# Kernel tuning notes

Hardware: AMD Instinct MI355X
Metric: run time of the kernel (lower is better)

## Reference

```python
import jax, jax.numpy as jnp
import numpy as np

TEMP = 1.75   # temp_schedule(epoch=5, warmup=10): 2.5 - 1.5*0.5
ALPHA = 0.5   # blend_schedule(epoch=5): 0.2 + 0.6*0.5
EPS = 1e-5
HEADS = 2


def _ln(x, g, b):
    mu = x.mean(-1, keepdims=True)
    var = ((x - mu) ** 2).mean(-1, keepdims=True)
    return (x - mu) * jax.lax.rsqrt(var + EPS) * g + b


def _gelu(x):
    return jax.nn.gelu(x, approximate=False)  # torch nn.GELU default = exact erf


def _attn_pool(x, ln_g, ln_b, in_w, in_b, out_w, out_b):
    # x: [N, T, E]; nn.MultiheadAttention self-attention then mean over T
    N, T, E = x.shape
    Dh = E // HEADS
    xn = _ln(x, ln_g, ln_b)
    qkv = xn @ in_w + in_b                      # [N, T, 3E] (in_w stored [E, 3E])
    q, k, v = jnp.split(qkv, 3, axis=-1)
    q = q.reshape(N, T, HEADS, Dh).transpose(0, 2, 1, 3)
    k = k.reshape(N, T, HEADS, Dh).transpose(0, 2, 1, 3)
    v = v.reshape(N, T, HEADS, Dh).transpose(0, 2, 1, 3)
    scores = jnp.einsum('nhqd,nhkd->nhqk', q, k) / jnp.sqrt(jnp.float32(Dh))
    a = jax.nn.softmax(scores, axis=-1)
    o = jnp.einsum('nhqk,nhkd->nhqd', a, v).transpose(0, 2, 1, 3).reshape(N, T, E)
    o = o @ out_w + out_b                       # [N, T, E]
    return o.mean(axis=1)                       # [N, E]


def setup_inputs() -> dict:
    key = jax.random.key(0)
    ks = iter(jax.random.split(key, 40))
    B, L, T, D = 4, 24, 400, 1024
    H = D // 2  # 512
    G = 4       # groups
    s = 0.02
    r = lambda shp: jax.random.normal(next(ks), shp, dtype=jnp.float32) * s
    inp = {
        'x': jax.random.normal(next(ks), (B, L, T, D), dtype=jnp.float32),
        'mlp_alpha': jnp.ones((L,), jnp.float32),
        # shared MLP: LN -> Linear(D,H) -> GELU -> Linear(H,H)
        's_ln_g': jnp.ones((D,), jnp.float32), 's_ln_b': jnp.zeros((D,), jnp.float32),
        's_w1': r((D, H)), 's_b1': jnp.zeros((H,), jnp.float32),
        's_w2': r((H, H)), 's_b2': jnp.zeros((H,), jnp.float32),
        # 4 group MLPs (stacked)
        'g_ln_g': jnp.ones((G, D), jnp.float32), 'g_ln_b': jnp.zeros((G, D), jnp.float32),
        'g_w1': r((G, D, H)), 'g_b1': jnp.zeros((G, H), jnp.float32),
        'g_w2': r((G, H, H)), 'g_b2': jnp.zeros((G, H), jnp.float32),
        # TimeAttentionPool (shared module): LN + MHA(512, 2 heads) + out_proj
        'p_ln_g': jnp.ones((H,), jnp.float32), 'p_ln_b': jnp.zeros((H,), jnp.float32),
        'p_in_w': r((H, 3 * H)), 'p_in_b': jnp.zeros((3 * H,), jnp.float32),
        'p_out_w': r((H, H)), 'p_out_b': jnp.zeros((H,), jnp.float32),
        # router: Linear(512,128) -> GELU -> Linear(128,1) -> sigmoid(/temp)
        'r_w1': r((H, 128)), 'r_b1': jnp.zeros((128,), jnp.float32),
        'r_w2': r((128, 1)), 'r_b2': jnp.zeros((1,), jnp.float32),
        # post norms
        'pn_g': jnp.ones((H,), jnp.float32), 'pn_b': jnp.zeros((H,), jnp.float32),
        'pnf_g': jnp.ones((H,), jnp.float32), 'pnf_b': jnp.zeros((H,), jnp.float32),
        # classifier 512 -> 256 -> 128 -> 2
        'c_w1': r((H, H // 2)), 'c_b1': jnp.zeros((H // 2,), jnp.float32),
        'c_w2': r((H // 2, H // 4)), 'c_b2': jnp.zeros((H // 4,), jnp.float32),
        'c_w3': r((H // 4, 2)), 'c_b3': jnp.zeros((2,), jnp.float32),
    }
    return inp


def reference(x, mlp_alpha, s_ln_g, s_ln_b, s_w1, s_b1, s_w2, s_b2,
              g_ln_g, g_ln_b, g_w1, g_b1, g_w2, g_b2,
              p_ln_g, p_ln_b, p_in_w, p_in_b, p_out_w, p_out_b,
              r_w1, r_b1, r_w2, r_b2, pn_g, pn_b, pnf_g, pnf_b,
              c_w1, c_b1, c_w2, c_b2, c_w3, c_b3):
    B, L, T, D = x.shape
    G = g_w1.shape[0]
    S = L // G  # group_size = 6; expert i uses group i // S
    H = s_w1.shape[1]

    # shared MLP over all experts at once (dropout inactive in eval)
    xs = _ln(x, s_ln_g, s_ln_b)                              # [B,L,T,D]
    shared = _gelu(xs @ s_w1 + s_b1) @ s_w2 + s_b2           # [B,L,T,H]

    # group MLPs: experts i//S -> group; reshape L -> (G, S)
    xg = x.reshape(B, G, S, T, D)
    xgn = _ln(xg, g_ln_g[:, None, None, :], g_ln_b[:, None, None, :])
    hg = _gelu(jnp.einsum('bgstd,gdh->bgsth', xgn, g_w1) + g_b1[None, :, None, None, :])
    grp = jnp.einsum('bgsth,ghk->bgstk', hg, g_w2) + g_b2[None, :, None, None, :]
    grp = grp.reshape(B, L, T, H)

    weighted = shared + mlp_alpha[None, :, None, None] * grp  # [B,L,T,H]

    # attn-pool every expert stream (fold L into batch)
    time_pooled = _attn_pool(weighted.reshape(B * L, T, H),
                             p_ln_g, p_ln_b, p_in_w, p_in_b, p_out_w, p_out_b)
    time_pooled = time_pooled.reshape(B, L, H)               # [B,L,H]

    # router
    rh = _gelu(time_pooled @ r_w1 + r_b1)
    logits_r = (rh @ r_w2 + r_b2)[..., 0]                    # [B,L]
    learned = jax.nn.sigmoid(logits_r / TEMP)
    routing_weights = ALPHA * learned + (1.0 - ALPHA) / L

    # soft fusion over experts
    fusion = (weighted * routing_weights[:, :, None, None]).sum(axis=1)  # [B,T,H]
    fusion = _ln(fusion, pn_g, pn_b).mean(axis=1)            # [B,H]

    shared_mean = shared.mean(axis=1)                        # [B,T,H]
    time_ctx = _attn_pool(shared_mean, p_ln_g, p_ln_b, p_in_w, p_in_b, p_out_w, p_out_b)

    fused_all = _ln(fusion, pnf_g, pnf_b) + _ln(time_ctx, pnf_g, pnf_b)  # [B,H]

    h = _gelu(fused_all @ c_w1 + c_b1)
    h = _gelu(h @ c_w2 + c_b2)
    logits = h @ c_w3 + c_b3                                 # [B,2]
    return logits, routing_weights, fused_all, time_pooled
```

## Files before the change

kernel.cpp:

```cpp
#include <hip/hip_runtime.h>
#include <stdint.h>


typedef float f32x4 __attribute__((ext_vector_type(4)));
typedef short bf16x8 __attribute__((ext_vector_type(8)));

__device__ __forceinline__ float bf2f(unsigned short u) {
  return __uint_as_float(((unsigned int)u) << 16);
}
__device__ __forceinline__ unsigned short f2bf(float f) {
  unsigned int u = __float_as_uint(f);
  u += 0x7fffu + ((u >> 16) & 1u);
  return (unsigned short)(u >> 16);
}
__device__ __forceinline__ float erf_fast(float x) {
  const float ax = fabsf(x);
  const float t = 1.0f / fmaf(0.3275911f, ax, 1.0f);
  float p = fmaf(1.061405429f, t, -1.453152027f);
  p = fmaf(p, t, 1.421413741f);
  p = fmaf(p, t, -0.284496736f);
  p = fmaf(p, t, 0.254829592f);
  const float e = __expf(-ax * ax);
  const float r = 1.0f - p * t * e;
  return copysignf(r, x);
}
__device__ __forceinline__ float gelu_f(float x) {
  return 0.5f * x * (1.0f + erf_fast(x * 0.70710678118654752440f));
}

typedef __attribute__((address_space(1))) const unsigned int gas_u32;
typedef __attribute__((address_space(3))) unsigned int las_u32;
__device__ __forceinline__ void gload16(const unsigned short* g, unsigned short* l) {
  __builtin_amdgcn_global_load_lds((gas_u32*)g, (las_u32*)l, 16, 0, 0);
}

template <int EPI, int GROUPED>
__global__ __launch_bounds__(256, 4) void gemm_bt(
    const unsigned short* __restrict__ A, const unsigned short* __restrict__ WT,
    const float* __restrict__ bias, unsigned short* __restrict__ Cout,
    const unsigned short* __restrict__ WT2, const float* __restrict__ bias2,
    const float* __restrict__ alpha_vec, unsigned short* __restrict__ vtbuf, int K,
    int N, int ldout, int Mslice) {
  const int tid = (int)threadIdx.x;
  const int w = tid >> 6, lane = tid & 63, g = lane >> 4, ql = lane & 15;
  const int wr = w >> 1, wc = w & 1;

  int bm, bn, z = 0;
  if (!GROUPED) {
    const int nbm = (int)gridDim.x, nbn = (int)gridDim.y;
    const int nb = nbm * nbn;
    const int lin = (int)blockIdx.x + nbm * (int)blockIdx.y;
    const int q = nb >> 3, r8 = nb & 7;
    const int xcd = lin & 7, c = lin >> 3;
    const int base = (xcd < r8) ? xcd * (q + 1) : r8 * (q + 1) + (xcd - r8) * q;
    const int widx = base + c;
    bm = widx / nbn;
    bn = widx - bm * nbn;
  } else {
    const int nbm = (int)gridDim.x, nbn = (int)gridDim.y;
    const int per_z = nbm * nbn;
    const int nb = per_z * (int)gridDim.z;
    const int lin =
        (int)blockIdx.x + nbm * ((int)blockIdx.y + (int)gridDim.y * (int)blockIdx.z);
    const int q = nb >> 3, r8 = nb & 7;
    const int xcd = lin & 7, c = lin >> 3;
    const int base = (xcd < r8) ? xcd * (q + 1) : r8 * (q + 1) + (xcd - r8) * q;
    const int widx = base + c;
    z = widx / per_z;
    const int rem = widx - z * per_z;
    bm = rem / nbn;
    bn = rem - bm * nbn;
  }
  const int n0 = bn * 128;

  int rowbase, rows_here;
  int nw0 = n0;
  const unsigned short* wt = WT;
  const float* bs = bias;
  if (GROUPED) {
    const int grp = z & 3;
    rowbase = z * Mslice + bm * 128;
    rows_here = Mslice - bm * 128;
    if (rows_here > 128) rows_here = 128;
    if (EPI == 4) {
      if (bn >= 4) {
        wt = WT2 + (size_t)grp * 512 * (size_t)K;
        bs = bias2 + (size_t)grp * 512;
        nw0 = n0 - 512;
      }
    } else if (EPI == 5) {
      wt = WT + (size_t)grp * (size_t)N * (size_t)K;
    } else {
      wt = WT + (size_t)grp * (size_t)N * (size_t)K;
      bs = bias + (size_t)grp * (size_t)N;
    }
  } else {
    rowbase = bm * 128;
    rows_here = Mslice - bm * 128;
    if (rows_here > 128) rows_here = 128;
  }

  __shared__ __align__(16) unsigned short sA[2][128 * 32];
  __shared__ __align__(16) unsigned short sB[2][128 * 32];

  f32x4 acc[4][4];
#pragma unroll
  for (int i = 0; i < 4; ++i)
#pragma unroll
    for (int j = 0; j < 4; ++j) acc[i][j] = (f32x4){0.f, 0.f, 0.f, 0.f};

  const int swzg = (lane & 3) ^ ((lane >> 3) & 3);
  const int rA0 = w * 32 + (lane >> 2);
  const int rA1 = rA0 + 16;
  const int rA0c = rA0 < rows_here ? rA0 : rows_here - 1;
  const int rA1c = rA1 < rows_here ? rA1 : rows_here - 1;
  const unsigned short* a0p = A + (size_t)(rowbase + rA0c) * K + swzg * 8;
  const unsigned short* a1p = A + (size_t)(rowbase + rA1c) * K + swzg * 8;
  const unsigned short* b0p = wt + (size_t)(nw0 + rA0) * K + swzg * 8;
  const unsigned short* b1p = wt + (size_t)(nw0 + rA1) * K + swzg * 8;
  const int ldsw = w * 1024;

  const int aroff = (wr * 64 + ql) * 32 + ((g ^ ((ql >> 1) & 3)) * 8);
  const int broff = (wc * 64 + ql) * 32 + ((g ^ ((ql >> 1) & 3)) * 8);

  const int nsteps = K >> 5;
  gload16(a0p, &sA[0][ldsw]);
  gload16(a1p, &sA[0][ldsw + 512]);
  gload16(b0p, &sB[0][ldsw]);
  gload16(b1p, &sB[0][ldsw + 512]);
  __syncthreads();

  for (int s = 0; s < nsteps; ++s) {
    const int cur = s & 1;
    if (s + 1 < nsteps) {
      const int k0 = (s + 1) << 5;
      const int nxt = cur ^ 1;
      gload16(a0p + k0, &sA[nxt][ldsw]);
      gload16(a1p + k0, &sA[nxt][ldsw + 512]);
      gload16(b0p + k0, &sB[nxt][ldsw]);
      gload16(b1p + k0, &sB[nxt][ldsw + 512]);
    }
    bf16x8 af[4], bfr[4];
#pragma unroll
    for (int mi = 0; mi < 4; ++mi)
      af[mi] = *(const bf16x8*)(&sA[cur][aroff + mi * 512]);
#pragma unroll
    for (int ni = 0; ni < 4; ++ni)
      bfr[ni] = *(const bf16x8*)(&sB[cur][broff + ni * 512]);
#pragma unroll
    for (int mi = 0; mi < 4; ++mi)
#pragma unroll
      for (int ni = 0; ni < 4; ++ni)
        acc[mi][ni] =
            __builtin_amdgcn_mfma_f32_16x16x32_bf16(af[mi], bfr[ni], acc[mi][ni], 0, 0, 0);
    __syncthreads();
  }

#pragma unroll
  for (int mi = 0; mi < 4; ++mi) {
#pragma unroll
    for (int r = 0; r < 4; ++r) {
      const int rloc = wr * 64 + mi * 16 + 4 * g + r;
      if (rloc >= rows_here) continue;
      const int grow = rowbase + rloc;
      float alpha_r = 1.f;
      const float* b2row = bias2;
      if (GROUPED && (EPI == 4 || EPI == 5)) {
        const int l_idx = (grow / 400) % 24;
        if (EPI == 5) b2row = bias2 + (size_t)l_idx * 512;
        if (EPI == 4) alpha_r = alpha_vec[l_idx];
      }
#pragma unroll
      for (int ni = 0; ni < 4; ++ni) {
        const int col = n0 + wc * 64 + ni * 16 + ql;
        const int colw = (EPI == 4 && bn >= 4) ? (col - 512) : col;
        float v;
        if (EPI == 5) {
          v = acc[mi][ni][r] + b2row[col];
        } else {
          v = acc[mi][ni][r] + bs[colw];
        }
        if (EPI == 1 || EPI == 4) v = gelu_f(v);
        if (EPI == 4 && bn >= 4) v *= alpha_r;
        if (EPI == 3) {
          if (col < 1024) {
            Cout[(size_t)grow * ldout + col] = f2bf(v);
          } else {
            vtbuf[(size_t)grow * 512 + (col - 1024)] = f2bf(v);
          }
        } else {
          Cout[(size_t)grow * ldout + col] = f2bf(v);
        }
      }
    }
  }
}

__global__ void transpose_v(const unsigned short* __restrict__ vbuf,
                            unsigned short* __restrict__ vt) {
  const int p = blockIdx.z;
  const int h = p & 1, nst = p >> 1;
  const int t0 = blockIdx.x * 32, d0 = blockIdx.y * 32;
  __shared__ unsigned short tile[32][33];
  const int tx = threadIdx.x, ty = threadIdx.y;
#pragma unroll
  for (int i = 0; i < 4; ++i) {
    const int t = t0 + ty + i * 8;
    if (t < 400)
      tile[ty + i * 8][tx] = vbuf[((size_t)nst * 400 + t) * 512 + h * 256 + d0 + tx];
  }
  __syncthreads();
  const int t = t0 + tx;
  if (t < 400) {
#pragma unroll
    for (int i = 0; i < 4; ++i)
      vt[((size_t)p * 256 + d0 + ty + i * 8) * 400 + t] = tile[tx][ty + i * 8];
  }
}

__global__ __launch_bounds__(256, 2) void attn_fwd(const unsigned short* __restrict__ qk,
                                                   const unsigned short* __restrict__ vt,
                                                   unsigned short* __restrict__ outb) {
  const int nb = (int)gridDim.x;
  int flat = (int)blockIdx.x;
  flat = (flat & 7) * (nb >> 3) + (flat >> 3);
  const int qt = flat % 7;
  const int h = (flat / 7) & 1;
  const int n = flat / 14;
  const int q0 = qt * 64;

  const int tid = (int)threadIdx.x;
  const int w = tid >> 6, lane = tid & 63, g = lane >> 4, ql = lane & 15;

  __shared__ __align__(16) unsigned short slab[400 * 32];
  __shared__ __align__(16) unsigned short Pc[4][512];
  __shared__ float rs[4][16];

  const int qr = q0 + w * 16 + ql;
  const int qrc = qr < 400 ? qr : 399;
  const unsigned short* qp = qk + ((size_t)n * 400 + qrc) * 1024 + h * 256 + g * 8;
  bf16x8 qf[8];
#pragma unroll
  for (int d0 = 0; d0 < 8; ++d0) qf[d0] = *(const bf16x8*)(qp + d0 * 32);

  f32x4 st[25];
#pragma unroll
  for (int kf = 0; kf < 25; ++kf) st[kf] = (f32x4){0.f, 0.f, 0.f, 0.f};

  const unsigned short* kbase = qk + (size_t)n * 400 * 1024 + 512 + h * 256;
  for (int d0 = 0; d0 < 8; ++d0) {
    bf16x8 stg[7];
#pragma unroll
    for (int c = 0; c < 7; ++c) {
      const int q = tid + c * 256;
      const int r = q >> 2, slot = q & 3;
      if (r < 400)
        stg[c] = *(const bf16x8*)(kbase + (size_t)r * 1024 + d0 * 32 + slot * 8);
    }
    __syncthreads();
#pragma unroll
    for (int c = 0; c < 7; ++c) {
      const int q = tid + c * 256;
      const int r = q >> 2, slot = q & 3;
      if (r < 400) *(bf16x8*)(slab + r * 32 + (slot ^ ((r >> 1) & 3)) * 8) = stg[c];
    }
    __syncthreads();
#pragma unroll
    for (int kf = 0; kf < 25; ++kf) {
      const int r = kf * 16 + ql;
      bf16x8 kfr = *(const bf16x8*)(slab + r * 32 + ((g ^ ((r >> 1) & 3)) * 8));
      st[kf] = __builtin_amdgcn_mfma_f32_16x16x32_bf16(kfr, qf[d0], st[kf], 0, 0, 0);
    }
  }

  const float sc = 0.0625f;
  float m = -3.0e38f;
#pragma unroll
  for (int kf = 0; kf < 25; ++kf)
    m = fmaxf(m, fmaxf(fmaxf(st[kf][0], st[kf][1]), fmaxf(st[kf][2], st[kf][3])));
  m = fmaxf(m, __shfl_xor(m, 16));
  m = fmaxf(m, __shfl_xor(m, 32));
  float sum = 0.f;
  uint2 pp[25];
#pragma unroll
  for (int kf = 0; kf < 25; ++kf) {
    float e0 = __expf((st[kf][0] - m) * sc);
    float e1 = __expf((st[kf][1] - m) * sc);
    float e2 = __expf((st[kf][2] - m) * sc);
    float e3 = __expf((st[kf][3] - m) * sc);
    sum += (e0 + e1) + (e2 + e3);
    pp[kf].x = (unsigned int)f2bf(e0) | ((unsigned int)f2bf(e1) << 16);
    pp[kf].y = (unsigned int)f2bf(e2) | ((unsigned int)f2bf(e3) << 16);
  }
  sum += __shfl_xor(sum, 16);
  sum += __shfl_xor(sum, 32);
  if (g == 0) rs[w][ql] = sum;

  f32x4 oacc[16];
#pragma unroll
  for (int nf = 0; nf < 16; ++nf) oacc[nf] = (f32x4){0.f, 0.f, 0.f, 0.f};

  unsigned short* Pw = Pc[w];
  const unsigned short* vbase = vt + (size_t)(n * 2 + h) * 256 * 400;
  for (int kt = 0; kt < 13; ++kt) {
    const int k0 = kt * 32;
    bf16x8 stg[4];
#pragma unroll
    for (int c = 0; c < 4; ++c) {
      const int q = tid + c * 256;
      const int r = q >> 2, slot = q & 3;
      int kc = k0 + slot * 8;
      if (kc >= 400) kc = 0;
      stg[c] = *(const bf16x8*)(vbase + (size_t)r * 400 + kc);
    }
    __syncthreads();
#pragma unroll
    for (int c = 0; c < 4; ++c) {
      const int q = tid + c * 256;
      const int r = q >> 2, slot = q & 3;
      *(bf16x8*)(slab + r * 32 + (slot ^ ((r >> 1) & 3)) * 8) = stg[c];
    }
    {
      const int kf0 = 2 * kt;
      *(uint2*)(Pw + ql * 32 + 4 * g) = pp[kf0];
      uint2 hi = (kf0 + 1 < 25) ? pp[kf0 + 1] : (uint2){0u, 0u};
      *(uint2*)(Pw + ql * 32 + 16 + 4 * g) = hi;
    }
    __syncthreads();
    bf16x8 pa = *(const bf16x8*)(Pw + ql * 32 + g * 8);
#pragma unroll
    for (int nf = 0; nf < 16; ++nf) {
      const int r = nf * 16 + ql;
      bf16x8 vb = *(const bf16x8*)(slab + r * 32 + ((g ^ ((r >> 1) & 3)) * 8));
      oacc[nf] = __builtin_amdgcn_mfma_f32_16x16x32_bf16(pa, vb, oacc[nf], 0, 0, 0);
    }
  }

  const float inv0 = 1.f / rs[w][4 * g + 0];
  const float inv1 = 1.f / rs[w][4 * g + 1];
  const float inv2 = 1.f / rs[w][4 * g + 2];
  const float inv3 = 1.f / rs[w][4 * g + 3];
#pragma unroll
  for (int nf = 0; nf < 16; ++nf) {
#pragma unroll
    for (int r = 0; r < 4; ++r) {
      const int qrow = q0 + w * 16 + 4 * g + r;
      if (qrow < 400) {
        const float invr = (r == 0) ? inv0 : (r == 1) ? inv1 : (r == 2) ? inv2 : inv3;
        outb[((size_t)n * 400 + qrow) * 512 + h * 256 + nf * 16 + ql] =
            f2bf(oacc[nf][r] * invr);
      }
    }
  }
}

template <int TIN, int TOUT>
__global__ void ln_rows(const void* __restrict__ inv, void* __restrict__ outv,
                        const float* __restrict__ gam, const float* __restrict__ bet,
                        int C) {
  const int row = blockIdx.x, t = (int)threadIdx.x;
  float x0, x1, x2, x3;
  if (TIN == 0) {
    float4 v = ((const float4*)inv)[(size_t)row * (C >> 2) + t];
    x0 = v.x; x1 = v.y; x2 = v.z; x3 = v.w;
  } else {
    ushort4 v = ((const ushort4*)inv)[(size_t)row * (C >> 2) + t];
    x0 = bf2f(v.x); x1 = bf2f(v.y); x2 = bf2f(v.z); x3 = bf2f(v.w);
  }
  float s1 = x0 + x1 + x2 + x3;
  float s2 = x0 * x0 + x1 * x1 + x2 * x2 + x3 * x3;
  for (int mlane = 1; mlane < 64; mlane <<= 1) {
    s1 += __shfl_xor(s1, mlane);
    s2 += __shfl_xor(s2, mlane);
  }
  __shared__ float red[8];
  const int nw = blockDim.x >> 6;
  if ((t & 63) == 0) {
    red[t >> 6] = s1;
    red[4 + (t >> 6)] = s2;
  }
  __syncthreads();
  s1 = 0.f; s2 = 0.f;
  for (int i = 0; i < nw; ++i) {
    s1 += red[i];
    s2 += red[4 + i];
  }
  const float mu = s1 / C;
  const float var = s2 / C - mu * mu;
  const float rstd = rsqrtf(var + 1e-5f);
  float y0 = (x0 - mu) * rstd, y1 = (x1 - mu) * rstd, y2 = (x2 - mu) * rstd,
        y3 = (x3 - mu) * rstd;
  if (gam) {
    const int c = t * 4;
    y0 = y0 * gam[c + 0] + bet[c + 0];
    y1 = y1 * gam[c + 1] + bet[c + 1];
    y2 = y2 * gam[c + 2] + bet[c + 2];
    y3 = y3 * gam[c + 3] + bet[c + 3];
  }
  if (TOUT == 0) {
    ushort4 o;
    o.x = f2bf(y0); o.y = f2bf(y1); o.z = f2bf(y2); o.w = f2bf(y3);
    ((ushort4*)outv)[(size_t)row * (C >> 2) + t] = o;
  } else {
    float4 o;
    o.x = y0; o.y = y1; o.z = y2; o.w = y3;
    ((float4*)outv)[(size_t)row * (C >> 2) + t] = o;
  }
}

__global__ void transpose_w(const float* __restrict__ W, const float* __restrict__ scale,
                            unsigned short* __restrict__ WT, int K, int N) {
  __shared__ float tile[32][33];
  const int k0 = blockIdx.x * 32, n0 = blockIdx.y * 32, zg = blockIdx.z;
  const float* Wz = W + (size_t)zg * K * N;
  const float* sz = scale ? scale + (size_t)zg * K : (const float*)0;
  unsigned short* WTz = WT + (size_t)zg * (size_t)K * N;
  const int tx = threadIdx.x, ty = threadIdx.y;
#pragma unroll
  for (int i = 0; i < 4; ++i)
    tile[ty + i * 8][tx] = Wz[(size_t)(k0 + ty + i * 8) * N + n0 + tx];
  __syncthreads();
#pragma unroll
  for (int i = 0; i < 4; ++i) {
    const int nn = n0 + ty + i * 8;
    const int kk = k0 + tx;
    float v = tile[tx][ty + i * 8];
    if (sz) v *= sz[kk];
    WTz[(size_t)nn * K + kk] = f2bf(v);
  }
}

__global__ void transpose_wf(const float* __restrict__ W, float* __restrict__ WT, int K,
                             int N) {
  __shared__ float tile[32][33];
  const int k0 = blockIdx.x * 32, n0 = blockIdx.y * 32;
  const int tx = threadIdx.x, ty = threadIdx.y;
#pragma unroll
  for (int i = 0; i < 4; ++i) {
    const int k = k0 + ty + i * 8;
    if (k < K && n0 + tx < N) tile[ty + i * 8][tx] = W[(size_t)k * N + n0 + tx];
  }
  __syncthreads();
#pragma unroll
  for (int i = 0; i < 4; ++i) {
    const int nn = n0 + ty + i * 8;
    const int kk = k0 + tx;
    if (nn < N && kk < K) WT[(size_t)nn * K + kk] = tile[tx][ty + i * 8];
  }
}

__global__ void build_wcomb2(const unsigned short* __restrict__ sw2T,
                             const unsigned short* __restrict__ gw2T,
                             unsigned short* __restrict__ wc) {
  const int q = (int)blockIdx.x * 256 + (int)threadIdx.x;
  if (q >= 4 * 512 * 256) return;
  const int grp = q / (512 * 256);
  const int rem = q - grp * (512 * 256);
  const int n = rem >> 8, kq = rem & 255;
  ushort4 v;
  if (kq < 128) {
    v = ((const ushort4*)sw2T)[(size_t)n * 128 + kq];
  } else {
    v = ((const ushort4*)gw2T)[((size_t)grp * 512 + n) * 128 + (kq - 128)];
  }
  ((ushort4*)wc)[q] = v;
}

__global__ void build_beff2(const float* __restrict__ s_b2, const float* __restrict__ g_b2,
                            const float* __restrict__ alpha, float* __restrict__ beff2) {
  const int l = (int)blockIdx.x;
  const int n = (int)threadIdx.x;
  beff2[(size_t)l * 512 + n] = s_b2[n] + alpha[l] * g_b2[(size_t)(l / 6) * 512 + n];
}

#define BF_KC 64
__global__ void bias_fold_part(const float* __restrict__ W, const float* __restrict__ lb,
                               float* __restrict__ part, int K, int N) {
  const int zg = blockIdx.z;
  const int n = blockIdx.x * 256 + (int)threadIdx.x;
  const int kc = blockIdx.y;
  const int kpc = K / BF_KC;
  const float* Wz = W + (size_t)zg * K * N;
  const float* lbz = lb + (size_t)zg * K;
  float acc = 0.f;
  const int k1 = (kc + 1) * kpc;
  for (int k = kc * kpc; k < k1; ++k) acc += lbz[k] * Wz[(size_t)k * N + n];
  part[((size_t)zg * BF_KC + kc) * N + n] = acc;
}
__global__ void bias_fold_final(const float* __restrict__ part, const float* __restrict__ b,
                                float* __restrict__ beff, int N) {
  const int zg = blockIdx.y;
  const int n = blockIdx.x * 256 + (int)threadIdx.x;
  float acc = b[(size_t)zg * N + n];
#pragma unroll
  for (int c = 0; c < BF_KC; ++c) acc += part[((size_t)zg * BF_KC + c) * N + n];
  beff[(size_t)zg * N + n] = acc;
}

__global__ void mean_h(const unsigned short* __restrict__ h,
                       unsigned short* __restrict__ out) {
  const int i = blockIdx.x * 256 + (int)threadIdx.x;
  if (i >= 4 * 400 * 128) return;
  const int b = i / (400 * 128);
  const int rem = i - b * (400 * 128);
  const int t = rem >> 7, c4 = rem & 127;
  float a0 = 0.f, a1 = 0.f, a2 = 0.f, a3 = 0.f;
  for (int l = 0; l < 24; ++l) {
    ushort4 v = *(const ushort4*)(h + ((size_t)(b * 24 + l) * 400 + t) * 1024 + c4 * 4);
    a0 += bf2f(v.x); a1 += bf2f(v.y); a2 += bf2f(v.z); a3 += bf2f(v.w);
  }
  ushort4 o;
  o.x = f2bf(a0 * (1.f / 24.f));
  o.y = f2bf(a1 * (1.f / 24.f));
  o.z = f2bf(a2 * (1.f / 24.f));
  o.w = f2bf(a3 * (1.f / 24.f));
  *(ushort4*)(out + ((size_t)(b * 400 + t)) * 512 + c4 * 4) = o;
}

template <int TIN>
__global__ void mean_t_part(const void* __restrict__ inv, float* __restrict__ part,
                            int Ns) {
  const int bx = (int)blockIdx.x;
  const int n = bx >> 2, cb = bx & 3;
  const int p = (int)blockIdx.y;
  const int c = cb * 128 + (int)threadIdx.x;
  float acc = 0.f;
  const int t0 = p * 50;
  if (TIN) {
    const unsigned short* in = (const unsigned short*)inv;
    for (int t = t0; t < t0 + 50; ++t) acc += bf2f(in[((size_t)n * 400 + t) * 512 + c]);
  } else {
    const float* in = (const float*)inv;
    for (int t = t0; t < t0 + 50; ++t) acc += in[((size_t)n * 400 + t) * 512 + c];
  }
  part[((size_t)p * Ns + n) * 512 + c] = acc;
}
__global__ void mean_t_fin(const float* __restrict__ part, float* __restrict__ out,
                           int Ns) {
  const int i = (int)blockIdx.x * 256 + (int)threadIdx.x;
  if (i >= Ns * 512) return;
  const int n = i >> 9, c = i & 511;
  float acc = 0.f;
#pragma unroll
  for (int p = 0; p < 8; ++p) acc += part[((size_t)p * Ns + n) * 512 + c];
  out[i] = acc * (1.f / 400.f);
}

__global__ void fuse_ln(const unsigned short* __restrict__ wgt,
                        const float* __restrict__ rw, const float* __restrict__ gam,
                        const float* __restrict__ bet, float* __restrict__ fln) {
  const int row = (int)blockIdx.x;
  const int b = row / 400, tt = row - b * 400;
  const int t = (int)threadIdx.x;
  float a0 = 0.f, a1 = 0.f, a2 = 0.f, a3 = 0.f;
  for (int l = 0; l < 24; ++l) {
    const float wv = rw[b * 24 + l];
    ushort4 v = *(const ushort4*)(wgt + ((size_t)(b * 24 + l) * 400 + tt) * 512 + t * 4);
    a0 += wv * bf2f(v.x); a1 += wv * bf2f(v.y);
    a2 += wv * bf2f(v.z); a3 += wv * bf2f(v.w);
  }
  float s1 = a0 + a1 + a2 + a3;
  float s2 = a0 * a0 + a1 * a1 + a2 * a2 + a3 * a3;
  for (int mlane = 1; mlane < 64; mlane <<= 1) {
    s1 += __shfl_xor(s1, mlane);
    s2 += __shfl_xor(s2, mlane);
  }
  __shared__ float red[4];
  if ((t & 63) == 0) {
    red[t >> 6] = s1;
    red[2 + (t >> 6)] = s2;
  }
  __syncthreads();
  s1 = red[0] + red[1];
  s2 = red[2] + red[3];
  const float mu = s1 * (1.f / 512.f);
  const float var = s2 * (1.f / 512.f) - mu * mu;
  const float rstd = rsqrtf(var + 1e-5f);
  const int c = t * 4;
  float4 o;
  o.x = (a0 - mu) * rstd * gam[c + 0] + bet[c + 0];
  o.y = (a1 - mu) * rstd * gam[c + 1] + bet[c + 1];
  o.z = (a2 - mu) * rstd * gam[c + 2] + bet[c + 2];
  o.w = (a3 - mu) * rstd * gam[c + 3] + bet[c + 3];
  ((float4*)fln)[(size_t)row * 128 + t] = o;
}

__global__ void ln2_add(const float* __restrict__ a, const float* __restrict__ bsrc,
                        const float* __restrict__ gam, const float* __restrict__ bet,
                        float* __restrict__ o1, float* __restrict__ o2) {
  const int row = (int)blockIdx.x;
  const int t = (int)threadIdx.x;
  float4 av = ((const float4*)a)[(size_t)row * 128 + t];
  float4 bv = ((const float4*)bsrc)[(size_t)row * 128 + t];
  float s1a = av.x + av.y + av.z + av.w;
  float s2a = av.x * av.x + av.y * av.y + av.z * av.z + av.w * av.w;
  float s1b = bv.x + bv.y + bv.z + bv.w;
  float s2b = bv.x * bv.x + bv.y * bv.y + bv.z * bv.z + bv.w * bv.w;
  for (int mlane = 1; mlane < 64; mlane <<= 1) {
    s1a += __shfl_xor(s1a, mlane);
    s2a += __shfl_xor(s2a, mlane);
    s1b += __shfl_xor(s1b, mlane);
    s2b += __shfl_xor(s2b, mlane);
  }
  __shared__ float red[8];
  if ((t & 63) == 0) {
    const int wv = t >> 6;
    red[wv] = s1a; red[2 + wv] = s2a; red[4 + wv] = s1b; red[6 + wv] = s2b;
  }
  __syncthreads();
  s1a = red[0] + red[1]; s2a = red[2] + red[3];
  s1b = red[4] + red[5]; s2b = red[6] + red[7];
  const float mua = s1a * (1.f / 512.f);
  const float ra = rsqrtf(s2a * (1.f / 512.f) - mua * mua + 1e-5f);
  const float mub = s1b * (1.f / 512.f);
  const float rb = rsqrtf(s2b * (1.f / 512.f) - mub * mub + 1e-5f);
  const int c = t * 4;
  float4 o;
  o.x = ((av.x - mua) * ra * gam[c + 0] + bet[c + 0]) +
        ((bv.x - mub) * rb * gam[c + 0] + bet[c + 0]);
  o.y = ((av.y - mua) * ra * gam[c + 1] + bet[c + 1]) +
        ((bv.y - mub) * rb * gam[c + 1] + bet[c + 1]);
  o.z = ((av.z - mua) * ra * gam[c + 2] + bet[c + 2]) +
        ((bv.z - mub) * rb * gam[c + 2] + bet[c + 2]);
  o.w = ((av.w - mua) * ra * gam[c + 3] + bet[c + 3]) +
        ((bv.w - mub) * rb * gam[c + 3] + bet[c + 3]);
  ((float4*)o1)[(size_t)row * 128 + t] = o;
  ((float4*)o2)[(size_t)row * 128 + t] = o;
}

template <int WLAYOUT>
__global__ void gemv_wave(const float* __restrict__ A, const float* __restrict__ Wm,
                          const float* __restrict__ b, float* __restrict__ C, int M, int K,
                          int N, int act) {
  const int wid = (int)(blockIdx.x * (blockDim.x >> 6)) + ((int)threadIdx.x >> 6);
  const int lane = (int)threadIdx.x & 63;
  if (wid >= M * N) return;
  const int row = wid / N, col = wid - row * N;
  const float* a = A + (size_t)row * K;
  float acc = 0.f;
  if (WLAYOUT) {
    const float* wt = Wm + (size_t)col * K;
    for (int k = lane; k < K; k += 64) acc += a[k] * wt[k];
  } else {
    for (int k = lane; k < K; k += 64) acc += a[k] * Wm[(size_t)k * N + col];
  }
#pragma unroll
  for (int d = 1; d < 64; d <<= 1) acc += __shfl_xor(acc, d);
  if (lane == 0) {
    acc += b[col];
    if (act) acc = gelu_f(acc);
    C[wid] = acc;
  }
}

__global__ void routing_k(const float* __restrict__ lr, float* __restrict__ o1,
                          float* __restrict__ o2) {
  const int i = (int)threadIdx.x;
  if (i < 96) {
    const float v = 0.5f / (1.f + __expf(-lr[i] * (1.f / 1.75f))) + (0.5f / 24.f);
    o1[i] = v;
    o2[i] = v;
  }
}

extern "C" void kernel_launch(void* const* d_in, const int* in_sizes, int n_in,
                              void* d_out, int out_size, void* d_ws, size_t ws_size,
                              hipStream_t stream) {
  const float* x = (const float*)d_in[0];
  const float* mlp_alpha = (const float*)d_in[1];
  const float* s_ln_g = (const float*)d_in[2];
  const float* s_ln_b = (const float*)d_in[3];
  const float* s_w1 = (const float*)d_in[4];
  const float* s_b1 = (const float*)d_in[5];
  const float* s_w2 = (const float*)d_in[6];
  const float* s_b2 = (const float*)d_in[7];
  const float* g_ln_g = (const float*)d_in[8];
  const float* g_ln_b = (const float*)d_in[9];
  const float* g_w1 = (const float*)d_in[10];
  const float* g_b1 = (const float*)d_in[11];
  const float* g_w2 = (const float*)d_in[12];
  const float* g_b2 = (const float*)d_in[13];
  const float* p_ln_g = (const float*)d_in[14];
  const float* p_ln_b = (const float*)d_in[15];
  const float* p_in_w = (const float*)d_in[16];
  const float* p_in_b = (const float*)d_in[17];
  const float* p_out_w = (const float*)d_in[18];
  const float* p_out_b = (const float*)d_in[19];
  const float* r_w1 = (const float*)d_in[20];
  const float* r_b1 = (const float*)d_in[21];
  const float* r_w2 = (const float*)d_in[22];
  const float* r_b2 = (const float*)d_in[23];
  const float* pn_g = (const float*)d_in[24];
  const float* pn_b = (const float*)d_in[25];
  const float* pnf_g = (const float*)d_in[26];
  const float* pnf_b = (const float*)d_in[27];
  const float* c_w1 = (const float*)d_in[28];
  const float* c_b1 = (const float*)d_in[29];
  const float* c_w2 = (const float*)d_in[30];
  const float* c_b2 = (const float*)d_in[31];
  const float* c_w3 = (const float*)d_in[32];
  const float* c_b3 = (const float*)d_in[33];

  float* out = (float*)d_out;
  uint8_t* ws = (uint8_t*)d_ws;

  size_t off = 0;
  auto alloc = [&](size_t bytes) -> size_t {
    size_t o = off;
    off += (bytes + 255) & ~(size_t)255;
    return o;
  };
  const size_t off_xhat = alloc(38400ull * 1024 * 2);
  const size_t off_h = alloc(38400ull * 1024 * 2);
  const size_t off_weighted = alloc(38400ull * 512 * 2);
  const size_t off_qk = alloc(38400ull * 1024 * 2);
  const size_t off_pooled = alloc(96ull * 512 * 4);
  const size_t off_rh = alloc(96ull * 128 * 4);
  const size_t off_lr = alloc(96ull * 4);
  const size_t off_rw = alloc(96ull * 4);
  const size_t off_hmean = alloc(1600ull * 512 * 2);
  const size_t off_smb = alloc(1600ull * 512 * 2);
  const size_t off_wn2 = alloc(1600ull * 512 * 2);
  const size_t off_qk2 = alloc(1600ull * 1024 * 2);
  const size_t off_vbuf2 = alloc(1600ull * 512 * 2);
  const size_t off_vt2 = alloc(4ull * 2 * 256 * 400 * 2);
  const size_t off_ao2 = alloc(1600ull * 512 * 2);
  const size_t off_pooled2 = alloc(4ull * 512 * 4);
  const size_t off_tctx = alloc(4ull * 512 * 4);
  const size_t off_fln = alloc(4ull * 400 * 512 * 4);
  const size_t off_fvec = alloc(4ull * 512 * 4);
  const size_t off_fall = alloc(4ull * 512 * 4);
  const size_t off_c1 = alloc(4ull * 256 * 4);
  const size_t off_c2 = alloc(4ull * 128 * 4);
  const size_t off_sw1T = alloc(512ull * 1024 * 2);
  const size_t off_sw2T = alloc(512ull * 512 * 2);
  const size_t off_gw1T = alloc(4ull * 512 * 1024 * 2);
  const size_t off_gw2T = alloc(4ull * 512 * 512 * 2);
  const size_t off_pinT = alloc(1536ull * 512 * 2);
  const size_t off_wc2 = alloc(4ull * 512 * 1024 * 2);
  const size_t off_sb1e = alloc(512ull * 4);
  const size_t off_gb1e = alloc(4ull * 512 * 4);
  const size_t off_pinbe = alloc(1536ull * 4);
  const size_t off_beff2 = alloc(24ull * 512 * 4);
  const size_t off_bfp_s = alloc((size_t)BF_KC * 512 * 4);
  const size_t off_bfp_g = alloc(4ull * BF_KC * 512 * 4);
  const size_t off_bfp_p = alloc((size_t)BF_KC * 1536 * 4);
  const size_t off_powT = alloc(512ull * 512 * 4);
  const size_t off_rw1T = alloc(128ull * 512 * 4);
  const size_t off_cw1T = alloc(256ull * 512 * 4);
  const size_t off_cw2T = alloc(128ull * 256 * 4);
  const size_t off_mtp = alloc(8ull * 96 * 512 * 4);
  const size_t off_wn = off_xhat;
  const size_t off_vbuf = off_xhat + 38400ull * 512 * 2;
  const size_t off_ao = off_h;
  const size_t off_vt = off_h + 38400ull * 512 * 2;
  if (off > ws_size) return;

  unsigned short* xhat = (unsigned short*)(ws + off_xhat);
  unsigned short* hbuf = (unsigned short*)(ws + off_h);
  unsigned short* weighted = (unsigned short*)(ws + off_weighted);
  unsigned short* qk = (unsigned short*)(ws + off_qk);
  unsigned short* wn = (unsigned short*)(ws + off_wn);
  unsigned short* vbuf = (unsigned short*)(ws + off_vbuf);
  unsigned short* vt = (unsigned short*)(ws + off_vt);
  unsigned short* ao = (unsigned short*)(ws + off_ao);
  float* pooled = (float*)(ws + off_pooled);
  float* rh = (float*)(ws + off_rh);
  float* lr = (float*)(ws + off_lr);
  float* rw = (float*)(ws + off_rw);
  unsigned short* hmean_b = (unsigned short*)(ws + off_hmean);
  unsigned short* smean_b = (unsigned short*)(ws + off_smb);
  unsigned short* wn2 = (unsigned short*)(ws + off_wn2);
  unsigned short* qk2 = (unsigned short*)(ws + off_qk2);
  unsigned short* vbuf2 = (unsigned short*)(ws + off_vbuf2);
  unsigned short* vt2 = (unsigned short*)(ws + off_vt2);
  unsigned short* ao2 = (unsigned short*)(ws + off_ao2);
  float* pooled2 = (float*)(ws + off_pooled2);
  float* tctx = (float*)(ws + off_tctx);
  float* fln = (float*)(ws + off_fln);
  float* fvec = (float*)(ws + off_fvec);
  float* fall = (float*)(ws + off_fall);
  float* c1 = (float*)(ws + off_c1);
  float* c2 = (float*)(ws + off_c2);
  unsigned short* sw1T = (unsigned short*)(ws + off_sw1T);
  unsigned short* sw2T = (unsigned short*)(ws + off_sw2T);
  unsigned short* gw1T = (unsigned short*)(ws + off_gw1T);
  unsigned short* gw2T = (unsigned short*)(ws + off_gw2T);
  unsigned short* pinT = (unsigned short*)(ws + off_pinT);
  unsigned short* wcomb2 = (unsigned short*)(ws + off_wc2);
  float* sb1e = (float*)(ws + off_sb1e);
  float* gb1e = (float*)(ws + off_gb1e);
  float* pinbe = (float*)(ws + off_pinbe);
  float* beff2 = (float*)(ws + off_beff2);
  float* bfp_s = (float*)(ws + off_bfp_s);
  float* bfp_g = (float*)(ws + off_bfp_g);
  float* bfp_p = (float*)(ws + off_bfp_p);
  float* powT = (float*)(ws + off_powT);
  float* rw1T = (float*)(ws + off_rw1T);
  float* cw1T = (float*)(ws + off_cw1T);
  float* cw2T = (float*)(ws + off_cw2T);
  float* mtp = (float*)(ws + off_mtp);

  transpose_w<<<dim3(32, 16, 1), dim3(32, 8), 0, stream>>>(s_w1, s_ln_g, sw1T, 1024, 512);
  transpose_w<<<dim3(16, 16, 1), dim3(32, 8), 0, stream>>>(s_w2, (const float*)0, sw2T, 512, 512);
  transpose_w<<<dim3(32, 16, 4), dim3(32, 8), 0, stream>>>(g_w1, g_ln_g, gw1T, 1024, 512);
  transpose_w<<<dim3(16, 16, 4), dim3(32, 8), 0, stream>>>(g_w2, (const float*)0, gw2T, 512, 512);
  transpose_w<<<dim3(16, 48, 1), dim3(32, 8), 0, stream>>>(p_in_w, p_ln_g, pinT, 512, 1536);
  transpose_wf<<<dim3(16, 16), dim3(32, 8), 0, stream>>>(p_out_w, powT, 512, 512);
  transpose_wf<<<dim3(16, 4), dim3(32, 8), 0, stream>>>(r_w1, rw1T, 512, 128);
  transpose_wf<<<dim3(16, 8), dim3(32, 8), 0, stream>>>(c_w1, cw1T, 512, 256);
  transpose_wf<<<dim3(8, 4), dim3(32, 8), 0, stream>>>(c_w2, cw2T, 256, 128);
  build_wcomb2<<<2048, 256, 0, stream>>>(sw2T, gw2T, wcomb2);
  build_beff2<<<24, 512, 0, stream>>>(s_b2, g_b2, mlp_alpha, beff2);
  bias_fold_part<<<dim3(2, BF_KC, 1), 256, 0, stream>>>(s_w1, s_ln_b, bfp_s, 1024, 512);
  bias_fold_final<<<dim3(2, 1), 256, 0, stream>>>(bfp_s, s_b1, sb1e, 512);
  bias_fold_part<<<dim3(2, BF_KC, 4), 256, 0, stream>>>(g_w1, g_ln_b, bfp_g, 1024, 512);
  bias_fold_final<<<dim3(2, 4), 256, 0, stream>>>(bfp_g, g_b1, gb1e, 512);
  bias_fold_part<<<dim3(6, BF_KC, 1), 256, 0, stream>>>(p_in_w, p_ln_b, bfp_p, 512, 1536);
  bias_fold_final<<<dim3(6, 1), 256, 0, stream>>>(bfp_p, p_in_b, pinbe, 1536);

  ln_rows<0, 0><<<38400, 256, 0, stream>>>(x, xhat, (const float*)0, (const float*)0, 1024);

  gemm_bt<4, 1><<<dim3(19, 8, 16), 256, 0, stream>>>(xhat, sw1T, sb1e, hbuf, gw1T, gb1e,
      mlp_alpha, (unsigned short*)0, 1024, 1024, 1024, 2400);

  gemm_bt<5, 1><<<dim3(19, 4, 16), 256, 0, stream>>>(hbuf, wcomb2, (const float*)0,
      weighted, (const unsigned short*)0, beff2, (const float*)0, (unsigned short*)0,
      1024, 512, 512, 2400);

  mean_h<<<800, 256, 0, stream>>>(hbuf, hmean_b);
  gemm_bt<0, 0><<<dim3(13, 4, 1), 256, 0, stream>>>(hmean_b, sw2T, s_b2, smean_b,
      (const unsigned short*)0, (const float*)0, (const float*)0, (unsigned short*)0,
      512, 512, 512, 1600);

  ln_rows<1, 0><<<38400, 128, 0, stream>>>(weighted, wn, (const float*)0, (const float*)0, 512);
  gemm_bt<3, 0><<<dim3(300, 12, 1), 256, 0, stream>>>(wn, pinT, pinbe, qk,
      (const unsigned short*)0, (const float*)0, (const float*)0, vbuf, 512, 1536, 1024,
      38400);
  transpose_v<<<dim3(13, 8, 192), dim3(32, 8), 0, stream>>>(vbuf, vt);
  attn_fwd<<<dim3(14 * 96), 256, 0, stream>>>(qk, vt, ao);
  mean_t_part<1><<<dim3(96 * 4, 8), 128, 0, stream>>>(ao, mtp, 96);
  mean_t_fin<<<192, 256, 0, stream>>>(mtp, pooled, 96);
  gemv_wave<1><<<12288, 256, 0, stream>>>(pooled, powT, p_out_b, out + 2152, 96, 512, 512, 0);

  gemv_wave<1><<<3072, 256, 0, stream>>>(out + 2152, rw1T, r_b1, rh, 96, 512, 128, 1);
  gemv_wave<0><<<24, 256, 0, stream>>>(rh, r_w2, r_b2, lr, 96, 128, 1, 0);
  routing_k<<<1, 128, 0, stream>>>(lr, out + 8, rw);

  fuse_ln<<<1600, 128, 0, stream>>>(weighted, rw, pn_g, pn_b, fln);
  mean_t_part<0><<<dim3(4 * 4, 8), 128, 0, stream>>>(fln, mtp, 4);
  mean_t_fin<<<8, 256, 0, stream>>>(mtp, fvec, 4);

  ln_rows<1, 0><<<1600, 128, 0, stream>>>(smean_b, wn2, (const float*)0, (const float*)0, 512);
  gemm_bt<3, 0><<<dim3(13, 12, 1), 256, 0, stream>>>(wn2, pinT, pinbe, qk2,
      (const unsigned short*)0, (const float*)0, (const float*)0, vbuf2, 512, 1536, 1024,
      1600);
  transpose_v<<<dim3(13, 8, 8), dim3(32, 8), 0, stream>>>(vbuf2, vt2);
  attn_fwd<<<dim3(14 * 4), 256, 0, stream>>>(qk2, vt2, ao2);
  mean_t_part<1><<<dim3(4 * 4, 8), 128, 0, stream>>>(ao2, mtp, 4);
  mean_t_fin<<<8, 256, 0, stream>>>(mtp, pooled2, 4);
  gemv_wave<1><<<512, 256, 0, stream>>>(pooled2, powT, p_out_b, tctx, 4, 512, 512, 0);

  ln2_add<<<4, 128, 0, stream>>>(fvec, tctx, pnf_g, pnf_b, out + 104, fall);

  gemv_wave<1><<<256, 256, 0, stream>>>(fall, cw1T, c_b1, c1, 4, 512, 256, 1);
  gemv_wave<1><<<128, 256, 0, stream>>>(c1, cw2T, c_b2, c2, 4, 256, 128, 1);
  gemv_wave<0><<<2, 256, 0, stream>>>(c2, c_w3, c_b3, out, 4, 128, 2, 0);
}
```

Baseline: 737.4 us.

## Fold LN into QKV GEMM epilogue and fuse time-mean into attention

Replaces the LayerNorm pass that wrote a normalized bf16 copy of weighted with a row-stats kernel. The mean/rstd correction is applied in a new GEMM epilogue using precomputed column sums of the QKV weight. The attention kernel now reduces its output over query rows in shared memory and writes per-tile partial sums. A small pool_fin kernel finishes the mean, so the full attention output tensor and the separate mean kernels are no longer needed. This trades extra epilogue arithmetic for much less memory traffic. It also risks some precision loss because the GEMM now runs on unnormalized bf16 inputs.

Result: faster. 720.8 us, median of 2 (-2.2%).

```diff
diff --git a/kernel.cpp b/kernel.cpp
--- a/kernel.cpp
+++ b/kernel.cpp
@@ -164,12 +164,18 @@
       if (rloc >= rows_here) continue;
       const int grow = rowbase + rloc;
       float alpha_r = 1.f;
+      float mu_r = 0.f, rstd_r = 1.f;
       const float* b2row = bias2;
       if (GROUPED && (EPI == 4 || EPI == 5)) {
         const int l_idx = (grow / 400) % 24;
         if (EPI == 5) b2row = bias2 + (size_t)l_idx * 512;
         if (EPI == 4) alpha_r = alpha_vec[l_idx];
       }
+      if (EPI == 6) {
+        const float2 strow = ((const float2*)bias2)[grow];
+        mu_r = strow.x;
+        rstd_r = strow.y;
+      }
 #pragma unroll
       for (int ni = 0; ni < 4; ++ni) {
         const int col = n0 + wc * 64 + ni * 16 + ql;
@@ -177,12 +183,14 @@
         float v;
         if (EPI == 5) {
           v = acc[mi][ni][r] + b2row[col];
+        } else if (EPI == 6) {
+          v = rstd_r * acc[mi][ni][r] + (bs[col] - rstd_r * mu_r * alpha_vec[col]);
         } else {
           v = acc[mi][ni][r] + bs[colw];
         }
         if (EPI == 1 || EPI == 4) v = gelu_f(v);
         if (EPI == 4 && bn >= 4) v *= alpha_r;
-        if (EPI == 3) {
+        if (EPI == 3 || EPI == 6) {
           if (col < 1024) {
             Cout[(size_t)grow * ldout + col] = f2bf(v);
           } else {
@@ -220,7 +228,7 @@
 
 __global__ __launch_bounds__(256, 2) void attn_fwd(const unsigned short* __restrict__ qk,
                                                    const unsigned short* __restrict__ vt,
-                                                   unsigned short* __restrict__ outb) {
+                                                   float* __restrict__ pool_part) {
   const int nb = (int)gridDim.x;
   int flat = (int)blockIdx.x;
   flat = (flat & 7) * (nb >> 3) + (flat >> 3);
@@ -235,6 +243,7 @@
   __shared__ __align__(16) unsigned short slab[400 * 32];
   __shared__ __align__(16) unsigned short Pc[4][512];
   __shared__ float rs[4][16];
+  __shared__ float psum[4][256];
 
   const int qr = q0 + w * 16 + ql;
   const int qrc = qr < 400 ? qr : 399;
@@ -340,18 +349,76 @@
   const float inv1 = 1.f / rs[w][4 * g + 1];
   const float inv2 = 1.f / rs[w][4 * g + 2];
   const float inv3 = 1.f / rs[w][4 * g + 3];
+
 #pragma unroll
   for (int nf = 0; nf < 16; ++nf) {
+    float s = 0.f;
 #pragma unroll
     for (int r = 0; r < 4; ++r) {
       const int qrow = q0 + w * 16 + 4 * g + r;
-      if (qrow < 400) {
-        const float invr = (r == 0) ? inv0 : (r == 1) ? inv1 : (r == 2) ? inv2 : inv3;
-        outb[((size_t)n * 400 + qrow) * 512 + h * 256 + nf * 16 + ql] =
-            f2bf(oacc[nf][r] * invr);
-      }
-    }
-  }
+      const float invr = (r == 0) ? inv0 : (r == 1) ? inv1 : (r == 2) ? inv2 : inv3;
+      if (qrow < 400) s += oacc[nf][r] * invr;
+    }
+    s += __shfl_xor(s, 16);
+    s += __shfl_xor(s, 32);
+    if (lane < 16) psum[w][nf * 16 + ql] = s;
+  }
+  __syncthreads();
+  if (tid < 256) {
+    const float s = psum[0][tid] + psum[1][tid] + psum[2][tid] + psum[3][tid];
+    pool_part[((size_t)((n * 2 + h) * 7 + qt)) * 256 + tid] = s;
+  }
+}
+
+__global__ void pool_fin(const float* __restrict__ part, float* __restrict__ out,
+                         int Ns) {
+  const int i = (int)blockIdx.x * 256 + (int)threadIdx.x;
+  if (i >= Ns * 512) return;
+  const int n = i >> 9, c = i & 511;
+  const int h = c >> 8, d = c & 255;
+  float s = 0.f;
+#pragma unroll
+  for (int qt = 0; qt < 7; ++qt)
+    s += part[((size_t)((n * 2 + h) * 7 + qt)) * 256 + d];
+  out[i] = s * (1.f / 400.f);
+}
+
+__global__ void row_stats(const unsigned short* __restrict__ in,
+                          float2* __restrict__ st) {
+  const int row = (int)blockIdx.x;
+  const int t = (int)threadIdx.x;
+  ushort4 v = ((const ushort4*)in)[(size_t)row * 128 + t];
+  const float x0 = bf2f(v.x), x1 = bf2f(v.y), x2 = bf2f(v.z), x3 = bf2f(v.w);
+  float s1 = x0 + x1 + x2 + x3;
+  float s2 = x0 * x0 + x1 * x1 + x2 * x2 + x3 * x3;
+  for (int mlane = 1; mlane < 64; mlane <<= 1) {
+    s1 += __shfl_xor(s1, mlane);
+    s2 += __shfl_xor(s2, mlane);
+  }
+  __shared__ float red[4];
+  if ((t & 63) == 0) {
+    red[t >> 6] = s1;
+    red[2 + (t >> 6)] = s2;
+  }
+  __syncthreads();
+  if (t == 0) {
+    s1 = red[0] + red[1];
+    s2 = red[2] + red[3];
+    const float mu = s1 * (1.f / 512.f);
+    const float var = s2 * (1.f / 512.f) - mu * mu;
+    st[row] = make_float2(mu, rsqrtf(var + 1e-5f));
+  }
+}
+
+__global__ void row_sum_bf16(const unsigned short* __restrict__ wm,
+                             float* __restrict__ out, int K) {
+  const int wid = (int)blockIdx.x * 4 + ((int)threadIdx.x >> 6);
+  const int lane = (int)threadIdx.x & 63;
+  float s = 0.f;
+  for (int k = lane; k < K; k += 64) s += bf2f(wm[(size_t)wid * K + k]);
+#pragma unroll
+  for (int d = 1; d < 64; d <<= 1) s += __shfl_xor(s, d);
+  if (lane == 0) out[wid] = s;
 }
 
 template <int TIN, int TOUT>
@@ -724,7 +791,6 @@
   const size_t off_qk2 = alloc(1600ull * 1024 * 2);
   const size_t off_vbuf2 = alloc(1600ull * 512 * 2);
   const size_t off_vt2 = alloc(4ull * 2 * 256 * 400 * 2);
-  const size_t off_ao2 = alloc(1600ull * 512 * 2);
   const size_t off_pooled2 = alloc(4ull * 512 * 4);
   const size_t off_tctx = alloc(4ull * 512 * 4);
   const size_t off_fln = alloc(4ull * 400 * 512 * 4);
@@ -750,9 +816,11 @@
   const size_t off_cw1T = alloc(256ull * 512 * 4);
   const size_t off_cw2T = alloc(128ull * 256 * 4);
   const size_t off_mtp = alloc(8ull * 96 * 512 * 4);
-  const size_t off_wn = off_xhat;
+  const size_t off_wstats = alloc(38400ull * 8);
+  const size_t off_csp = alloc(1536ull * 4);
+  const size_t off_pp1 = alloc(96ull * 14 * 256 * 4);
+  const size_t off_pp2 = alloc(4ull * 14 * 256 * 4);
   const size_t off_vbuf = off_xhat + 38400ull * 512 * 2;
-  const size_t off_ao = off_h;
   const size_t off_vt = off_h + 38400ull * 512 * 2;
   if (off > ws_size) return;
 
@@ -760,10 +828,8 @@
   unsigned short* hbuf = (unsigned short*)(ws + off_h);
   unsigned short* weighted = (unsigned short*)(ws + off_weighted);
   unsigned short* qk = (unsigned short*)(ws + off_qk);
-  unsigned short* wn = (unsigned short*)(ws + off_wn);
   unsigned short* vbuf = (unsigned short*)(ws + off_vbuf);
   unsigned short* vt = (unsigned short*)(ws + off_vt);
-  unsigned short* ao = (unsigned short*)(ws + off_ao);
   float* pooled = (float*)(ws + off_pooled);
   float* rh = (float*)(ws + off_rh);
   float* lr = (float*)(ws + off_lr);
@@ -774,7 +840,6 @@
   unsigned short* qk2 = (unsigned short*)(ws + off_qk2);
   unsigned short* vbuf2 = (unsigned short*)(ws + off_vbuf2);
   unsigned short* vt2 = (unsigned short*)(ws + off_vt2);
-  unsigned short* ao2 = (unsigned short*)(ws + off_ao2);
   float* pooled2 = (float*)(ws + off_pooled2);
   float* tctx = (float*)(ws + off_tctx);
   float* fln = (float*)(ws + off_fln);
@@ -800,6 +865,10 @@
   float* cw1T = (float*)(ws + off_cw1T);
   float* cw2T = (float*)(ws + off_cw2T);
   float* mtp = (float*)(ws + off_mtp);
+  float2* wstats = (float2*)(ws + off_wstats);
+  float* csP = (float*)(ws + off_csp);
+  float* pp1 = (float*)(ws + off_pp1);
+  float* pp2 = (float*)(ws + off_pp2);
 
   transpose_w<<<dim3(32, 16, 1), dim3(32, 8), 0, stream>>>(s_w1, s_ln_g, sw1T, 1024, 512);
   transpose_w<<<dim3(16, 16, 1), dim3(32, 8), 0, stream>>>(s_w2, (const float*)0, sw2T, 512, 512);
@@ -812,6 +881,7 @@
   transpose_wf<<<dim3(8, 4), dim3(32, 8), 0, stream>>>(c_w2, cw2T, 256, 128);
   build_wcomb2<<<2048, 256, 0, stream>>>(sw2T, gw2T, wcomb2);
   build_beff2<<<24, 512, 0, stream>>>(s_b2, g_b2, mlp_alpha, beff2);
+  row_sum_bf16<<<384, 256, 0, stream>>>(pinT, csP, 512);
   bias_fold_part<<<dim3(2, BF_KC, 1), 256, 0, stream>>>(s_w1, s_ln_b, bfp_s, 1024, 512);
   bias_fold_final<<<dim3(2, 1), 256, 0, stream>>>(bfp_s, s_b1, sb1e, 512);
   bias_fold_part<<<dim3(2, BF_KC, 4), 256, 0, stream>>>(g_w1, g_ln_b, bfp_g, 1024, 512);
@@ -833,14 +903,13 @@
       (const unsigned short*)0, (const float*)0, (const float*)0, (unsigned short*)0,
       512, 512, 512, 1600);
 
-  ln_rows<1, 0><<<38400, 128, 0, stream>>>(weighted, wn, (const float*)0, (const float*)0, 512);
-  gemm_bt<3, 0><<<dim3(300, 12, 1), 256, 0, stream>>>(wn, pinT, pinbe, qk,
-      (const unsigned short*)0, (const float*)0, (const float*)0, vbuf, 512, 1536, 1024,
+  row_stats<<<38400, 128, 0, stream>>>(weighted, wstats);
+  gemm_bt<6, 0><<<dim3(300, 12, 1), 256, 0, stream>>>(weighted, pinT, pinbe, qk,
+      (const unsigned short*)0, (const float*)wstats, csP, vbuf, 512, 1536, 1024,
       38400);
   transpose_v<<<dim3(13, 8, 192), dim3(32, 8), 0, stream>>>(vbuf, vt);
-  attn_fwd<<<dim3(14 * 96), 256, 0, stream>>>(qk, vt, ao);
-  mean_t_part<1><<<dim3(96 * 4, 8), 128, 0, stream>>>(ao, mtp, 96);
-  mean_t_fin<<<192, 256, 0, stream>>>(mtp, pooled, 96);
+  attn_fwd<<<dim3(14 * 96), 256, 0, stream>>>(qk, vt, pp1);
+  pool_fin<<<192, 256, 0, stream>>>(pp1, pooled, 96);
   gemv_wave<1><<<12288, 256, 0, stream>>>(pooled, powT, p_out_b, out + 2152, 96, 512, 512, 0);
 
   gemv_wave<1><<<3072, 256, 0, stream>>>(out + 2152, rw1T, r_b1, rh, 96, 512, 128, 1);
@@ -856,9 +925,8 @@
       (const unsigned short*)0, (const float*)0, (const float*)0, vbuf2, 512, 1536, 1024,
       1600);
   transpose_v<<<dim3(13, 8, 8), dim3(32, 8), 0, stream>>>(vbuf2, vt2);
-  attn_fwd<<<dim3(14 * 4), 256, 0, stream>>>(qk2, vt2, ao2);
-  mean_t_part<1><<<dim3(4 * 4, 8), 128, 0, stream>>>(ao2, mtp, 4);
-  mean_t_fin<<<8, 256, 0, stream>>>(mtp, pooled2, 4);
+  attn_fwd<<<dim3(14 * 4), 256, 0, stream>>>(qk2, vt2, pp2);
+  pool_fin<<<8, 256, 0, stream>>>(pp2, pooled2, 4);
   gemv_wave<1><<<512, 256, 0, stream>>>(pooled2, powT, p_out_b, tctx, 4, 512, 512, 0);
 
   ln2_add<<<4, 128, 0, stream>>>(fvec, tctx, pnf_g, pnf_b, out + 104, fall);
```
